# Kernel optimization log

Hardware: AMD Instinct MI355X
Metric: run time of the kernel (lower is better)

The kernel has to match this reference:

```python
import jax, jax.numpy as jnp
from jax import lax
import numpy as np

# --- static config (from module defaults / chosen shapes) ---
B, C, Hc, Wc = 16, 65, 160, 160
CELL = 8
H, W = Hc * CELL, Wc * CELL
NUM_KP = 512                          # num_keypoints
NMS_R = 8                             # nms_radius -> 17x17 window
MARGIN = 16                           # border_margin
NEG_INF = jnp.float32(-1e30)


def setup_inputs() -> dict:
    key = jax.random.key(0)
    heatmap = jax.random.normal(key, (B, C, Hc, Wc), dtype=jnp.float32)
    return {"heatmap": heatmap}


def _decode(heatmap):
    # softmax over 65 bins, drop dustbin -> (B, 64, Hc, Wc)
    prob = jax.nn.softmax(heatmap, axis=1)[:, :CELL * CELL]
    # pixel-shuffle to full-res score map (B, H, W)
    sm = (prob.transpose(0, 2, 3, 1)                 # (B,Hc,Wc,64)
              .reshape(B, Hc, Wc, CELL, CELL)
              .transpose(0, 1, 3, 2, 4)              # (B,Hc,8,Wc,8)
              .reshape(B, H, W))
    # border masking (zero outside margin)
    border = jnp.zeros((H, W), jnp.float32).at[MARGIN:H - MARGIN, MARGIN:W - MARGIN].set(1.0)
    sm = sm * border
    # 3x3 avg pool, stride 1, pad 1 (count_include_pad=True -> divide by 9)
    sm = lax.reduce_window(sm, 0.0, lax.add, (1, 3, 3), (1, 1, 1),
                           [(0, 0), (1, 1), (1, 1)]) / 9.0
    # NMS on detached scores: 17x17 max pool, -inf padding
    sm_d = lax.stop_gradient(sm)
    k = 2 * NMS_R + 1
    local_max = lax.reduce_window(sm_d, NEG_INF, lax.max, (1, k, k), (1, 1, 1),
                                  [(0, 0), (NMS_R, NMS_R), (NMS_R, NMS_R)])
    nms_mask = sm_d == local_max
    # suppress border band r = max(nms_radius, border_margin)
    r = max(NMS_R, MARGIN)
    interior = jnp.zeros((H, W), bool).at[r:H - r, r:W - r].set(True)
    nms_mask = nms_mask & interior
    # fixed-size top-k over masked flattened map (non-maxima get -inf)
    masked = jnp.where(nms_mask, sm_d, NEG_INF).reshape(B, H * W)
    _, top_idx = lax.top_k(masked, NUM_KP)           # (B, K)
    scores = jnp.take_along_axis(sm.reshape(B, H * W), top_idx, axis=1)  # (B,K)
    y = (top_idx // W).astype(jnp.float32)
    x = (top_idx % W).astype(jnp.float32)
    kp = jnp.stack([x, y], axis=-1)                  # (B, K, 2) in (x, y) px
    kp_norm = kp / jnp.array([W - 1, H - 1], jnp.float32)
    return kp_norm, scores


def reference(heatmap):
    return _decode(heatmap)
```

## Files before the change

### kernel.cpp

```cpp
#include <hip/hip_runtime.h>
#include <float.h>
#include <math.h>

#define BATCH 16
#define CHANS 65
#define HC 160
#define WC 160
#define HH 1280
#define WW 1280
#define KP 512
#define CAP 8192

static __device__ __forceinline__ unsigned long long make_key(float f, unsigned idx) {
  unsigned u = __float_as_uint(f);
  u = (u & 0x80000000u) ? ~u : (u | 0x80000000u);
  return ((unsigned long long)(~u) << 32) | (unsigned long long)idx;
}
static __device__ __forceinline__ float key_score(unsigned long long key) {
  unsigned mk = ~(unsigned)(key >> 32);
  unsigned u = (mk & 0x80000000u) ? (mk & 0x7FFFFFFFu) : ~mk;
  return __uint_as_float(u);
}

__global__ __launch_bounds__(256) void k_softmax_shuffle(const float* __restrict__ hm,
                                                         float* __restrict__ sm) {
  int id = blockIdx.x * 256 + threadIdx.x;
  const int NC = HC * WC;
  int b = id / NC;
  int cell = id - b * NC;
  int hc = cell / WC;
  int wc = cell - hc * WC;
  float* orow = sm + (size_t)b * HH * WW + (size_t)(hc * 8) * WW + wc * 8;

  if (hc < 2 || hc >= HC - 2 || wc < 2 || wc >= WC - 2) {
    float4 z = make_float4(0.f, 0.f, 0.f, 0.f);
#pragma unroll
    for (int r = 0; r < 8; ++r) {
      *(float4*)(orow + (size_t)r * WW) = z;
      *(float4*)(orow + (size_t)r * WW + 4) = z;
    }
    return;
  }

  const float* ibase = hm + (size_t)b * CHANS * NC + cell;
  float v[CHANS];
  float m = -FLT_MAX;
#pragma unroll
  for (int c = 0; c < CHANS; ++c) {
    v[c] = ibase[(size_t)c * NC];
    m = fmaxf(m, v[c]);
  }
  float s = 0.f;
#pragma unroll
  for (int c = 0; c < CHANS; ++c) {
    float d = __fsub_rn(v[c], m);
    v[c] = (float)exp((double)d);
    s = __fadd_rn(s, v[c]);
  }
#pragma unroll
  for (int r = 0; r < 8; ++r) {
    float4 q0, q1;
    q0.x = __fdiv_rn(v[r*8+0], s); q0.y = __fdiv_rn(v[r*8+1], s);
    q0.z = __fdiv_rn(v[r*8+2], s); q0.w = __fdiv_rn(v[r*8+3], s);
    q1.x = __fdiv_rn(v[r*8+4], s); q1.y = __fdiv_rn(v[r*8+5], s);
    q1.z = __fdiv_rn(v[r*8+6], s); q1.w = __fdiv_rn(v[r*8+7], s);
    *(float4*)(orow + (size_t)r * WW)     = q0;
    *(float4*)(orow + (size_t)r * WW + 4) = q1;
  }
}

#define CHUNKS 156
__global__ __launch_bounds__(512) void k_avg_vmax_nms(const float* __restrict__ sm,
                                                      int* __restrict__ cnt,
                                                      unsigned long long* __restrict__ cand) {
  __shared__ float lv[8 * WW];
  __shared__ float la[8 * WW];
  __shared__ int scan[512];
  __shared__ int sbase;
  int wgid = (blockIdx.x & 7) * 312 + (blockIdx.x >> 3);
  int b = wgid / CHUNKS;
  int chunk = wgid % CHUNKS;
  int y0 = 16 + 8 * chunk;
  int tid = threadIdx.x;
  const float* base = sm + (size_t)b * HH * WW;

  if (tid < 320) {
    int x0 = tid * 4;
    float lf[3], rt[3];
    float4 c4[3];
    float4 mm[8];
#pragma unroll
    for (int k2 = 0; k2 < 26; ++k2) {
      const float* row = base + (size_t)(y0 - 9 + k2) * WW;
      int slot = k2 % 3;
      lf[slot] = (x0 > 0) ? row[x0 - 1] : 0.f;
      c4[slot] = *(const float4*)(row + x0);
      rt[slot] = (x0 + 4 < WW) ? row[x0 + 4] : 0.f;
      if (k2 >= 2) {
        int k = k2 - 10;
        float a0 = 0.f, a1 = 0.f, a2 = 0.f, a3 = 0.f;
#pragma unroll
        for (int d = 0; d < 3; ++d) {
          int sl = (k2 - 2 + d) % 3;
          float l = lf[sl], r = rt[sl];
          float4 c = c4[sl];
          a0 = __fadd_rn(__fadd_rn(__fadd_rn(a0, l),   c.x), c.y);
          a1 = __fadd_rn(__fadd_rn(__fadd_rn(a1, c.x), c.y), c.z);
          a2 = __fadd_rn(__fadd_rn(__fadd_rn(a2, c.y), c.z), c.w);
          a3 = __fadd_rn(__fadd_rn(__fadd_rn(a3, c.z), c.w), r);
        }
        float4 a4;
        a4.x = __fdiv_rn(a0, 9.0f); a4.y = __fdiv_rn(a1, 9.0f);
        a4.z = __fdiv_rn(a2, 9.0f); a4.w = __fdiv_rn(a3, 9.0f);
        if (k >= 0 && k < 8) *(float4*)(la + k * WW + x0) = a4;
#pragma unroll
        for (int rr = 0; rr < 8; ++rr) {
          if (k == rr - 8) mm[rr] = a4;
          else if (k > rr - 8 && k <= rr + 8) {
            mm[rr].x = fmaxf(mm[rr].x, a4.x); mm[rr].y = fmaxf(mm[rr].y, a4.y);
            mm[rr].z = fmaxf(mm[rr].z, a4.z); mm[rr].w = fmaxf(mm[rr].w, a4.w);
          }
        }
      }
    }
#pragma unroll
    for (int rr = 0; rr < 8; ++rr) *(float4*)(lv + rr * WW + x0) = mm[rr];
  }
  __syncthreads();

  unsigned msk0 = 0, msk1 = 0, msk2 = 0;
  int cntl = 0;
#pragma unroll
  for (int k = 0; k < 3; ++k) {
    int x = tid + 512 * k;
    if (x >= 16 && x < 1264) {
      unsigned m = 0;
#pragma unroll
      for (int rr = 0; rr < 8; ++rr) {
        const float* lrow = lv + rr * WW;
        float wm = lrow[x - 8];
#pragma unroll
        for (int j = 1; j < 17; ++j) wm = fmaxf(wm, lrow[x - 8 + j]);
        float c = la[rr * WW + x];
        if (c >= wm) { m |= (1u << rr); cntl++; }
      }
      if (k == 0) msk0 = m; else if (k == 1) msk1 = m; else msk2 = m;
    }
  }

  scan[tid] = cntl;
  __syncthreads();
  for (int off = 1; off < 512; off <<= 1) {
    int v = scan[tid];
    if (tid >= off) v += scan[tid - off];
    __syncthreads();
    scan[tid] = v;
    __syncthreads();
  }
  if (tid == 0) {
    int total = scan[511];
    sbase = total ? atomicAdd(&cnt[b * 16], total) : 0;
  }
  __syncthreads();
  int pos = sbase + scan[tid] - cntl;
#pragma unroll
  for (int k = 0; k < 3; ++k) {
    int x = tid + 512 * k;
    unsigned m = (k == 0) ? msk0 : (k == 1) ? msk1 : msk2;
    while (m) {
      int rr = __ffs(m) - 1;
      m &= m - 1u;
      float c = la[rr * WW + x];
      if (pos < CAP) cand[(size_t)b * CAP + pos] = make_key(c, (unsigned)((y0 + rr) * WW + x));
      pos++;
    }
  }
}

#define CE_ASC(A, B) { unsigned long long _x = s[A], _y = s[B]; \
                       if (_x > _y) { s[A] = _y; s[B] = _x; } }

__global__ __launch_bounds__(256) void k_sort_chunks(const int* __restrict__ cnt,
                                                     const unsigned long long* __restrict__ cand,
                                                     unsigned long long* __restrict__ srt) {
  __shared__ unsigned long long s[1024];
  int b = blockIdx.x >> 3;
  int c = blockIdx.x & 7;
  int tid = threadIdx.x;
  int raw = cnt[b * 16];
  int count = raw > CAP ? CAP : raw;
  int base = c * 1024;
  for (int i = tid; i < 1024; i += 256)
    s[i] = (base + i < count) ? cand[(size_t)b * CAP + base + i] : ~0ULL;
  __syncthreads();
  for (int k = 2; k <= 1024; k <<= 1) {
    for (int j = k >> 1; j > 0; j >>= 1) {
      for (int i = tid; i < 1024; i += 256) {
        int ixj = i ^ j;
        if (ixj > i) {
          unsigned long long a = s[i], d = s[ixj];
          bool up = ((i & k) == 0);
          if ((a > d) == up) { s[i] = d; s[ixj] = a; }
        }
      }
      __syncthreads();
    }
  }
  for (int i = tid; i < 1024; i += 256)
    srt[(size_t)b * CAP + base + i] = s[i];
}

__global__ __launch_bounds__(1024) void k_merge_topk(const int* __restrict__ cnt,
                                                     const unsigned long long* __restrict__ srt,
                                                     float* __restrict__ out) {
  __shared__ unsigned long long s[CAP];
  __shared__ unsigned flagw[32];
  int b = blockIdx.x;
  int tid = threadIdx.x;
  int raw = cnt[b * 16];
  int count = raw > CAP ? CAP : raw;
  if (tid < 32) flagw[tid] = 0;

#pragma unroll
  for (int c = 0; c < 8; ++c) {
    unsigned long long v = srt[(size_t)b * CAP + c * 1024 + tid];
    if (c & 1) s[c * 1024 + (1023 - tid)] = v;
    else       s[c * 1024 + tid]          = v;
  }
  __syncthreads();

#pragma unroll
  for (int r = 0; r < 4; ++r) { int i = r * 2048 + tid; CE_ASC(i, i + 1024); }
  __syncthreads();
  for (int j = 512; j >= 1; j >>= 1) {
    for (int t = tid; t < 2048; t += 1024) {
      int r = t >> 9, u = t & 511;
      int i = r * 2048 + (u / j) * (2 * j) + (u % j);
      CE_ASC(i, i + j);
    }
    __syncthreads();
  }
  {
    unsigned long long v1 = s[2048 + 1023 - tid];
    unsigned long long v2 = s[6144 + 1023 - tid];
    s[1024 + tid] = v1;
    s[5120 + tid] = v2;
  }
  __syncthreads();
#pragma unroll
  for (int r = 0; r < 2; ++r) { int i = r * 4096 + tid; CE_ASC(i, i + 1024); }
  __syncthreads();
  for (int j = 512; j >= 1; j >>= 1) {
    int r = tid >> 9, u = tid & 511;
    int i = r * 4096 + (u / j) * (2 * j) + (u % j);
    CE_ASC(i, i + j);
    __syncthreads();
  }
  s[1024 + tid] = s[4096 + 1023 - tid];
  __syncthreads();
  CE_ASC(tid, tid + 1024);
  __syncthreads();
  for (int j = 512; j >= 1; j >>= 1) {
    if (tid < 512) {
      int i = (tid / j) * (2 * j) + (tid % j);
      CE_ASC(i, i + j);
    }
    __syncthreads();
  }

  int lim = count < 520 ? count : 520;
  if (tid + 1 < lim) {
    unsigned u0 = ~(unsigned)(s[tid] >> 32);
    unsigned u1 = ~(unsigned)(s[tid + 1] >> 32);
    unsigned i0 = (unsigned)(s[tid] & 0xFFFFFFFFu);
    unsigned i1 = (unsigned)(s[tid + 1] & 0xFFFFFFFFu);
    if (u0 - u1 <= 1u && i0 > i1) atomicOr(&flagw[tid >> 5], 1u << (tid & 31));
  }
  __syncthreads();
  if (tid == 0) {
    int resume = 0;
    for (int w = 0; w < 17; ++w) {
      unsigned f = flagw[w];
      while (f) {
        int p = w * 32 + (__ffs(f) - 1);
        f &= f - 1u;
        if (p < resume) continue;
        int i = p;
        while (i + 1 < lim) {
          unsigned u0 = ~(unsigned)(s[i] >> 32);
          unsigned u1 = ~(unsigned)(s[i + 1] >> 32);
          unsigned i0 = (unsigned)(s[i] & 0xFFFFFFFFu);
          unsigned i1 = (unsigned)(s[i + 1] & 0xFFFFFFFFu);
          if (u0 - u1 <= 1u && i0 > i1) {
            unsigned long long t = s[i]; s[i] = s[i + 1]; s[i + 1] = t;
            ++i;
          } else break;
        }
        resume = i + 1;
      }
    }
  }
  __syncthreads();

  if (tid < KP) {
    if (tid < count) {
      unsigned long long key = s[tid];
      unsigned idx = (unsigned)(key & 0xFFFFFFFFu);
      float score = key_score(key);
      float xf = (float)(idx % WW);
      float yf = (float)(idx / WW);
      out[((size_t)b * KP + tid) * 2 + 0] = __fdiv_rn(xf, 1279.0f);
      out[((size_t)b * KP + tid) * 2 + 1] = __fdiv_rn(yf, 1279.0f);
      out[(size_t)BATCH * KP * 2 + (size_t)b * KP + tid] = score;
    } else {
      out[((size_t)b * KP + tid) * 2 + 0] = 2.0f;
      out[((size_t)b * KP + tid) * 2 + 1] = 2.0f;
      out[(size_t)BATCH * KP * 2 + (size_t)b * KP + tid] = 0.0f;
    }
    if (tid == 0 && raw > CAP) {
      out[((size_t)b * KP) * 2 + 0] = 3.0f;
      out[((size_t)b * KP) * 2 + 1] = 3.0f;
    }
  }
}

extern "C" void kernel_launch(void* const* d_in, const int* in_sizes, int n_in,
                              void* d_out, int out_size, void* d_ws, size_t ws_size,
                              hipStream_t stream) {
  const float* hm = (const float*)d_in[0];
  float* out = (float*)d_out;
  char* ws = (char*)d_ws;

  int* cnt = (int*)ws;
  unsigned long long* cand = (unsigned long long*)(ws + 1024);
  unsigned long long* srt  = cand + (size_t)BATCH * CAP;
  float* sm  = (float*)((char*)srt + (size_t)BATCH * CAP * 8);

  hipMemsetAsync(cnt, 0, 1024, stream);

  k_softmax_shuffle<<<BATCH * HC * WC / 256, 256, 0, stream>>>(hm, sm);
  k_avg_vmax_nms<<<BATCH * CHUNKS, 512, 0, stream>>>(sm, cnt, cand);
  k_sort_chunks<<<BATCH * 8, 256, 0, stream>>>(cnt, cand, srt);
  k_merge_topk<<<BATCH, 1024, 0, stream>>>(cnt, srt, out);
}
```

Before: 247.8 us.

## Shrink NMS block to 320 threads, wave-level scan, defer division by nine

```diff
diff --git a/kernel.cpp b/kernel.cpp
--- a/kernel.cpp
+++ b/kernel.cpp
@@ -70,21 +70,24 @@
 }
 
 #define CHUNKS 156
-__global__ __launch_bounds__(512) void k_avg_vmax_nms(const float* __restrict__ sm,
+#define LVW 1264
+#define LAW 1248
+__global__ __launch_bounds__(320) void k_avg_vmax_nms(const float* __restrict__ sm,
                                                       int* __restrict__ cnt,
                                                       unsigned long long* __restrict__ cand) {
-  __shared__ float lv[8 * WW];
-  __shared__ float la[8 * WW];
-  __shared__ int scan[512];
+  __shared__ float lv[8 * LVW];
+  __shared__ float la[8 * LAW];
+  __shared__ int wsum[5], woff[5];
   __shared__ int sbase;
   int wgid = (blockIdx.x & 7) * 312 + (blockIdx.x >> 3);
   int b = wgid / CHUNKS;
   int chunk = wgid % CHUNKS;
   int y0 = 16 + 8 * chunk;
   int tid = threadIdx.x;
+  int wv = tid >> 6, lane = tid & 63;
   const float* base = sm + (size_t)b * HH * WW;
 
-  if (tid < 320) {
+  {
     int x0 = tid * 4;
     float lf[3], rt[3];
     float4 c4[3];
@@ -109,68 +112,80 @@
           a2 = __fadd_rn(__fadd_rn(__fadd_rn(a2, c.y), c.z), c.w);
           a3 = __fadd_rn(__fadd_rn(__fadd_rn(a3, c.z), c.w), r);
         }
-        float4 a4;
-        a4.x = __fdiv_rn(a0, 9.0f); a4.y = __fdiv_rn(a1, 9.0f);
-        a4.z = __fdiv_rn(a2, 9.0f); a4.w = __fdiv_rn(a3, 9.0f);
-        if (k >= 0 && k < 8) *(float4*)(la + k * WW + x0) = a4;
+        float4 s4 = make_float4(a0, a1, a2, a3);
+        if (k >= 0 && k < 8 && x0 >= 16 && x0 <= 1260) {
+          float4 a4;
+          a4.x = __fdiv_rn(s4.x, 9.0f); a4.y = __fdiv_rn(s4.y, 9.0f);
+          a4.z = __fdiv_rn(s4.z, 9.0f); a4.w = __fdiv_rn(s4.w, 9.0f);
+          *(float4*)(la + k * LAW + (x0 - 16)) = a4;
+        }
 #pragma unroll
         for (int rr = 0; rr < 8; ++rr) {
-          if (k == rr - 8) mm[rr] = a4;
+          if (k == rr - 8) mm[rr] = s4;
           else if (k > rr - 8 && k <= rr + 8) {
-            mm[rr].x = fmaxf(mm[rr].x, a4.x); mm[rr].y = fmaxf(mm[rr].y, a4.y);
-            mm[rr].z = fmaxf(mm[rr].z, a4.z); mm[rr].w = fmaxf(mm[rr].w, a4.w);
+            mm[rr].x = fmaxf(mm[rr].x, s4.x); mm[rr].y = fmaxf(mm[rr].y, s4.y);
+            mm[rr].z = fmaxf(mm[rr].z, s4.z); mm[rr].w = fmaxf(mm[rr].w, s4.w);
           }
         }
       }
     }
-#pragma unroll
-    for (int rr = 0; rr < 8; ++rr) *(float4*)(lv + rr * WW + x0) = mm[rr];
-  }
-  __syncthreads();
-
-  unsigned msk0 = 0, msk1 = 0, msk2 = 0;
+    if (x0 >= 8 && x0 <= 1268) {
+#pragma unroll
+      for (int rr = 0; rr < 8; ++rr) {
+        float4 o;
+        o.x = __fdiv_rn(mm[rr].x, 9.0f); o.y = __fdiv_rn(mm[rr].y, 9.0f);
+        o.z = __fdiv_rn(mm[rr].z, 9.0f); o.w = __fdiv_rn(mm[rr].w, 9.0f);
+        *(float4*)(lv + rr * LVW + (x0 - 8)) = o;
+      }
+    }
+  }
+  __syncthreads();
+
+  unsigned msk0 = 0, msk1 = 0, msk2 = 0, msk3 = 0;
   int cntl = 0;
 #pragma unroll
-  for (int k = 0; k < 3; ++k) {
-    int x = tid + 512 * k;
-    if (x >= 16 && x < 1264) {
+  for (int k = 0; k < 4; ++k) {
+    int x = 16 + tid + 320 * k;
+    if (x < 1264) {
       unsigned m = 0;
 #pragma unroll
       for (int rr = 0; rr < 8; ++rr) {
-        const float* lrow = lv + rr * WW;
-        float wm = lrow[x - 8];
-#pragma unroll
-        for (int j = 1; j < 17; ++j) wm = fmaxf(wm, lrow[x - 8 + j]);
-        float c = la[rr * WW + x];
+        const float* lrow = lv + rr * LVW + (x - 16);
+        float wm = lrow[0];
+#pragma unroll
+        for (int j = 1; j < 17; ++j) wm = fmaxf(wm, lrow[j]);
+        float c = la[rr * LAW + (x - 16)];
         if (c >= wm) { m |= (1u << rr); cntl++; }
       }
-      if (k == 0) msk0 = m; else if (k == 1) msk1 = m; else msk2 = m;
-    }
-  }
-
-  scan[tid] = cntl;
-  __syncthreads();
-  for (int off = 1; off < 512; off <<= 1) {
-    int v = scan[tid];
-    if (tid >= off) v += scan[tid - off];
-    __syncthreads();
-    scan[tid] = v;
-    __syncthreads();
-  }
+      if (k == 0) msk0 = m; else if (k == 1) msk1 = m;
+      else if (k == 2) msk2 = m; else msk3 = m;
+    }
+  }
+
+  int inc = cntl;
+#pragma unroll
+  for (int off = 1; off < 64; off <<= 1) {
+    int t = __shfl_up(inc, off, 64);
+    if (lane >= off) inc += t;
+  }
+  if (lane == 63) wsum[wv] = inc;
+  __syncthreads();
   if (tid == 0) {
-    int total = scan[511];
-    sbase = total ? atomicAdd(&cnt[b * 16], total) : 0;
-  }
-  __syncthreads();
-  int pos = sbase + scan[tid] - cntl;
-#pragma unroll
-  for (int k = 0; k < 3; ++k) {
-    int x = tid + 512 * k;
-    unsigned m = (k == 0) ? msk0 : (k == 1) ? msk1 : msk2;
+    int acc = 0;
+#pragma unroll
+    for (int w = 0; w < 5; ++w) { woff[w] = acc; acc += wsum[w]; }
+    sbase = acc ? atomicAdd(&cnt[b * 16], acc) : 0;
+  }
+  __syncthreads();
+  int pos = sbase + woff[wv] + inc - cntl;
+#pragma unroll
+  for (int k = 0; k < 4; ++k) {
+    int x = 16 + tid + 320 * k;
+    unsigned m = (k == 0) ? msk0 : (k == 1) ? msk1 : (k == 2) ? msk2 : msk3;
     while (m) {
       int rr = __ffs(m) - 1;
       m &= m - 1u;
-      float c = la[rr * WW + x];
+      float c = la[rr * LAW + (x - 16)];
       if (pos < CAP) cand[(size_t)b * CAP + pos] = make_key(c, (unsigned)((y0 + rr) * WW + x));
       pos++;
     }
@@ -339,7 +354,7 @@
   hipMemsetAsync(cnt, 0, 1024, stream);
 
   k_softmax_shuffle<<<BATCH * HC * WC / 256, 256, 0, stream>>>(hm, sm);
-  k_avg_vmax_nms<<<BATCH * CHUNKS, 512, 0, stream>>>(sm, cnt, cand);
+  k_avg_vmax_nms<<<BATCH * CHUNKS, 320, 0, stream>>>(sm, cnt, cand);
   k_sort_chunks<<<BATCH * 8, 256, 0, stream>>>(cnt, cand, srt);
   k_merge_topk<<<BATCH, 1024, 0, stream>>>(cnt, srt, out);
 }
```

Result: faster. 237.4 us (-4.2%).
